# Kernel tuning notes

Measured on AMD Instinct MI355X. Metric: run time of the kernel, lower is better.

Reference implementation:

```python
import jax, jax.numpy as jnp
import numpy as np

D_MODEL = 256
NUM_HEADS = 8
D_HEAD = D_MODEL // NUM_HEADS


def setup_inputs() -> dict:
    key = jax.random.key(0)
    k1, k2, k3, k4, k5, k6 = jax.random.split(key, 6)
    B, L, C, H, W = 2, 2048, D_MODEL, 4, 4
    query = jax.random.normal(k1, (B, L, C, H, W), dtype=jnp.float32)
    key_t = jax.random.normal(k2, (B, L, C, H, W), dtype=jnp.float32)
    value = jax.random.normal(k3, (B, L, C, H, W), dtype=jnp.float32)
    # 1x1 conv weights (out_channels, in_channels), no bias
    s = 1.0 / np.sqrt(C)
    Wq = jax.random.uniform(k4, (C, C), jnp.float32, -s, s)
    Wk = jax.random.uniform(k5, (C, C), jnp.float32, -s, s)
    Wv = jax.random.uniform(k6, (C, C), jnp.float32, -s, s)
    return {"query": query, "key": key_t, "value": value, "Wq": Wq, "Wk": Wk, "Wv": Wv}


def _split_heads(x, B, L, H, W):
    # (B, L, C, H, W) -> (num_heads*B, L, d_head, H, W), head-major like torch permute(2,0,1,3,4,5)
    x = x.reshape(B, L, NUM_HEADS, D_HEAD, H, W)
    x = jnp.transpose(x, (2, 0, 1, 3, 4, 5))  # (nh, B, L, d_head, H, W)
    return x.reshape(NUM_HEADS * B, L, D_HEAD, H, W)


def reference(query, key, value, Wq, Wk, Wv):
    B, L, C, H, W = value.shape
    # 1x1 conv == channel matmul: (B,L,C,H,W) x (O,C) -> (B,L,O,H,W)
    q = jnp.einsum('blchw,oc->blohw', query, Wq)
    k = jnp.einsum('blchw,oc->blohw', key, Wk)
    v = jnp.einsum('blchw,oc->blohw', value, Wv)
    q = _split_heads(q, B, L, H, W)
    k = _split_heads(k, B, L, H, W)
    v = _split_heads(v, B, L, H, W)
    scale = 1.0 / np.sqrt(D_HEAD).astype(np.float32)
    score = jnp.einsum('bidhw,bjdhw->bij', q, k) * scale  # (nh*B, L, L)
    attn = jax.nn.softmax(score, axis=-1)
    context = jnp.einsum('bij,bjdhw->bidhw', attn, v)  # (nh*B, L, d_head, H, W)
    context = context.reshape(NUM_HEADS, B, L, D_HEAD, H, W)
    context = jnp.transpose(context, (1, 2, 0, 3, 4, 5)).reshape(B, L, C, H, W)
    return context, attn
```

## Files before the change

### kernel.cpp

```cpp
#include <hip/hip_runtime.h>


typedef short s16x8 __attribute__((ext_vector_type(8)));
typedef float f32x4 __attribute__((ext_vector_type(4)));

__device__ __forceinline__ unsigned short f2bf(float f) {
  union { float f; unsigned int u; } v; v.f = f;
  return (unsigned short)((v.u + 0x7FFFu + ((v.u >> 16) & 1u)) >> 16);
}
__device__ __forceinline__ float bf2f(unsigned short h) {
  union { unsigned int u; float f; } v; v.u = ((unsigned int)h) << 16;
  return v.f;
}

__device__ __forceinline__ void async_copy16(const unsigned short* g, unsigned short* l) {
  __builtin_amdgcn_global_load_lds((const __attribute__((address_space(1))) void*)g,
                                   (__attribute__((address_space(3))) void*)l, 16, 0, 0);
}


template <int LD>
__device__ __forceinline__ void stage256(const unsigned short* __restrict__ Xg,
                                         unsigned short* __restrict__ lds_base,
                                         int kt) {
  const int tid = threadIdx.x;
  const int wid = tid >> 6, lane = tid & 63;
  const int prow = lane >> 2, pgran = lane & 3;
  const int lgran = pgran ^ ((prow >> 1) & 3);
  const int row0 = wid * 32;
#pragma unroll
  for (int i = 0; i < 2; ++i) {
    const int rb = row0 + i * 16;
    async_copy16(Xg + (size_t)(rb + prow) * LD + kt * 32 + lgran * 8,
                 lds_base + rb * 32);
  }
}

__device__ __forceinline__ void compute256(const unsigned short* __restrict__ As_,
                                           const unsigned short* __restrict__ Bs_,
                                           f32x4 acc[8][4]) {
  const int tid = threadIdx.x, lane = tid & 63, wid = tid >> 6;
  const int wm = wid >> 2, wn = wid & 3;
  const int rl = lane & 15;
  const int xg = (lane >> 4) ^ ((rl >> 1) & 3);
  const unsigned short* Aw = As_ + (size_t)(wm * 128 + rl) * 32 + xg * 8;
  const unsigned short* Bw = Bs_ + (size_t)(wn * 64 + rl) * 32 + xg * 8;
  s16x8 b[4], a[4];
#pragma unroll
  for (int n = 0; n < 4; ++n) b[n] = *(const s16x8*)(Bw + n * 16 * 32);
#pragma unroll
  for (int m = 0; m < 4; ++m) a[m] = *(const s16x8*)(Aw + m * 16 * 32);
  __builtin_amdgcn_s_setprio(1);
#pragma unroll
  for (int m = 0; m < 4; ++m)
#pragma unroll
    for (int n = 0; n < 4; ++n)
      acc[m][n] = __builtin_amdgcn_mfma_f32_16x16x32_bf16(a[m], b[n], acc[m][n], 0, 0, 0);
  __builtin_amdgcn_s_setprio(0);
#pragma unroll
  for (int m = 0; m < 4; ++m) a[m] = *(const s16x8*)(Aw + (64 + m * 16) * 32);
  __builtin_amdgcn_s_setprio(1);
#pragma unroll
  for (int m = 0; m < 4; ++m)
#pragma unroll
    for (int n = 0; n < 4; ++n)
      acc[4 + m][n] = __builtin_amdgcn_mfma_f32_16x16x32_bf16(a[m], b[n], acc[4 + m][n], 0, 0, 0);
  __builtin_amdgcn_s_setprio(0);
}

template <int LD_A, int LD_B, int NT>
__device__ __forceinline__ void gemm256_loop(const unsigned short* __restrict__ Ag,
                                             const unsigned short* __restrict__ Bg,
                                             unsigned short (*As)[8192],
                                             unsigned short (*Bs)[8192],
                                             f32x4 acc[8][4]) {
  stage256<LD_A>(Ag, As[0], 0); stage256<LD_B>(Bg, Bs[0], 0);
  stage256<LD_A>(Ag, As[1], 1); stage256<LD_B>(Bg, Bs[1], 1);
  for (int kt = 0; kt < NT; ++kt) {
    if (kt < NT - 1) asm volatile("s_waitcnt vmcnt(4)" ::: "memory");
    else             asm volatile("s_waitcnt vmcnt(0)" ::: "memory");
    __builtin_amdgcn_s_barrier();
    compute256(As[kt & 1], Bs[kt & 1], acc);
    __builtin_amdgcn_s_barrier();
    if (kt + 2 < NT) {
      stage256<LD_A>(Ag, As[kt & 1], kt + 2);
      stage256<LD_B>(Bg, Bs[kt & 1], kt + 2);
    }
  }
}

#define ACC_INIT8(acc)                        \
  {                                           \
    const f32x4 z_ = {0.f, 0.f, 0.f, 0.f};    \
    _Pragma("unroll")                         \
    for (int m_ = 0; m_ < 8; ++m_)            \
      _Pragma("unroll")                       \
      for (int n_ = 0; n_ < 4; ++n_) acc[m_][n_] = z_; \
  }

__global__ void __launch_bounds__(512, 2)
gemm_proj_qk256_kernel(const unsigned short* __restrict__ Xq,
                       const unsigned short* __restrict__ Xk,
                       const unsigned short* __restrict__ Wbf,
                       unsigned short* __restrict__ q_s,
                       unsigned short* __restrict__ k_s) {
  __shared__ unsigned short As[2][8192], Bs[2][8192];
  f32x4 acc[8][4];
  ACC_INIT8(acc);
  const int z = blockIdx.z;
  const unsigned short* X = z ? Xk : Xq;
  const unsigned short* W = Wbf + z * 65536;
  unsigned short* out = z ? k_s : q_s;
  gemm256_loop<256, 256, 8>(X + (size_t)blockIdx.x * 256 * 256, W, As, Bs, acc);
  const int tid = threadIdx.x, lane = tid & 63, wid = tid >> 6;
  const int wm = wid >> 2, wn = wid & 3;
  const int R0 = blockIdx.x * 256 + wm * 128 + ((lane >> 4) << 2);
  const int C0 = wn * 64 + (lane & 15);
#pragma unroll
  for (int m = 0; m < 8; ++m)
#pragma unroll
    for (int n = 0; n < 4; ++n)
#pragma unroll
      for (int r = 0; r < 4; ++r) {
        int R = R0 + m * 16 + r;
        int o = C0 + n * 16;
        int bl = R >> 4, hw = R & 15;
        int b = bl >> 11, l = bl & 2047;
        int head = o >> 5, d = o & 31;
        out[((size_t)(head * 2 + b) * 2048 + l) * 512 + d * 16 + hw] = f2bf(acc[m][n][r]);
      }
}

__global__ void __launch_bounds__(512, 2)
gemm_proj_vt256_kernel(const unsigned short* __restrict__ W,
                       const unsigned short* __restrict__ X2,
                       unsigned short* __restrict__ vt) {
  __shared__ unsigned short As[2][8192], Bs[2][8192];
  f32x4 acc[8][4];
  ACC_INIT8(acc);
  gemm256_loop<256, 256, 8>(W, X2 + (size_t)blockIdx.x * 256 * 256, As, Bs, acc);
  const int tid = threadIdx.x, lane = tid & 63, wid = tid >> 6;
  const int wm = wid >> 2, wn = wid & 3;
  const int o0 = wm * 128 + ((lane >> 4) << 2);
  const int p0 = blockIdx.x * 256 + wn * 64 + (lane & 15);
#pragma unroll
  for (int m = 0; m < 8; ++m)
#pragma unroll
    for (int n = 0; n < 4; ++n)
#pragma unroll
      for (int r = 0; r < 4; ++r) {
        int o = o0 + m * 16 + r;
        int p = p0 + n * 16;
        int head = o >> 5, d = o & 31;
        int b = p >> 15, hw = (p >> 11) & 15, l = p & 2047;
        vt[((size_t)((head * 2 + b) * 512) + d * 16 + hw) * 2048 + l] = f2bf(acc[m][n][r]);
      }
}

__global__ void __launch_bounds__(512, 2)
gemm_score256_kernel(const unsigned short* __restrict__ q, const unsigned short* __restrict__ k,
                     unsigned short* __restrict__ pbf, float* __restrict__ partial) {
  __shared__ unsigned short As[2][8192], Bs[2][8192];
  f32x4 acc[8][4];
  ACC_INIT8(acc);
  const int bid = blockIdx.x;
  const int w_ = (bid & 7) * 128 + (bid >> 3);
  const int bx = w_ & 7, by = (w_ >> 3) & 7, bh = w_ >> 6;
  const unsigned short* Ag = q + ((size_t)bh * 2048 + bx * 256) * 512;
  const unsigned short* Bg = k + ((size_t)bh * 2048 + by * 256) * 512;
  gemm256_loop<512, 512, 16>(Ag, Bg, As, Bs, acc);
  const int tid = threadIdx.x, lane = tid & 63, wid = tid >> 6;
  const int wm = wid >> 2, wn = wid & 3;
  const float scale = 0.17677669529663687f;
  const int R0 = bx * 256 + wm * 128 + ((lane >> 4) << 2);
  const int C0 = by * 256 + wn * 64 + (lane & 15);
  unsigned short* P = pbf + (size_t)bh * 4194304;
#pragma unroll
  for (int m = 0; m < 8; ++m)
#pragma unroll
    for (int n = 0; n < 4; ++n)
#pragma unroll
      for (int r = 0; r < 4; ++r) {
        float e = __expf(acc[m][n][r] * scale);
        acc[m][n][r] = e;
        P[(size_t)(R0 + m * 16 + r) * 2048 + (C0 + n * 16)] = f2bf(e);
      }
  const int chunk = by * 4 + wn;
#pragma unroll
  for (int m = 0; m < 8; ++m)
#pragma unroll
    for (int r = 0; r < 4; ++r) {
      float s = (acc[m][0][r] + acc[m][1][r]) + (acc[m][2][r] + acc[m][3][r]);
      s += __shfl_xor(s, 1); s += __shfl_xor(s, 2);
      s += __shfl_xor(s, 4); s += __shfl_xor(s, 8);
      if ((lane & 15) == 0)
        partial[((size_t)bh * 2048 + R0 + m * 16 + r) * 32 + chunk] = s;
    }
}

__global__ void __launch_bounds__(512, 2)
gemm_ctx256_kernel(const unsigned short* __restrict__ pbf, const unsigned short* __restrict__ vt,
                   const float* __restrict__ inv_buf, float* __restrict__ outc) {
  __shared__ unsigned short As[2][8192], Bs[2][8192];
  f32x4 acc[8][4];
  ACC_INIT8(acc);
  const int bid = blockIdx.x;
  const int w_ = (bid & 7) * 32 + (bid >> 3);
  const int bx = w_ & 7, by = (w_ >> 3) & 1, bh = w_ >> 4;
  const unsigned short* Ag = pbf + (size_t)bh * 4194304 + (size_t)bx * 256 * 2048;
  const unsigned short* Bg = vt + (size_t)bh * 1048576 + (size_t)by * 256 * 2048;
  gemm256_loop<2048, 2048, 64>(Ag, Bg, As, Bs, acc);
  const int tid = threadIdx.x, lane = tid & 63, wid = tid >> 6;
  const int wm = wid >> 2, wn = wid & 3;
  const int b = bh & 1, head = bh >> 1;
  const int R0 = bx * 256 + wm * 128 + ((lane >> 4) << 2);
  const int C0 = by * 256 + wn * 64 + (lane & 15);
#pragma unroll
  for (int m = 0; m < 8; ++m)
#pragma unroll
    for (int r = 0; r < 4; ++r) {
      const int R = R0 + m * 16 + r;
      const float sc = inv_buf[(size_t)bh * 2048 + R];
#pragma unroll
      for (int n = 0; n < 4; ++n) {
        int dd = C0 + n * 16;
        outc[((size_t)(b * 2048 + R) * 256 + head * 32 + (dd >> 4)) * 16 + (dd & 15)] =
            acc[m][n][r] * sc;
      }
    }
}

__global__ void __launch_bounds__(256) prep_all_kernel(const float* __restrict__ qs,
                                                       const float* __restrict__ ks,
                                                       const float* __restrict__ vs,
                                                       unsigned short* __restrict__ Xq,
                                                       unsigned short* __restrict__ Xk,
                                                       unsigned short* __restrict__ X2) {
  __shared__ float ld[256 * 17];
  const int bl = blockIdx.x;
  const int z = blockIdx.y;
  const int t = threadIdx.x;
  const float* s = (z == 0 ? qs : (z == 1 ? ks : vs)) + (size_t)bl * 4096;
#pragma unroll
  for (int i = 0; i < 4; ++i) {
    int flat = i * 1024 + t * 4;
    float4 v = *(const float4*)(s + flat);
    int c = flat >> 4, hw = flat & 15;
    float* p = &ld[c * 17 + hw];
    p[0] = v.x; p[1] = v.y; p[2] = v.z; p[3] = v.w;
  }
  __syncthreads();
  if (z < 2) {
    unsigned short* d = (z == 0 ? Xq : Xk) + (size_t)bl * 4096;
#pragma unroll
    for (int hw = 0; hw < 16; ++hw)
      d[hw * 256 + t] = f2bf(ld[t * 17 + hw]);
  } else {
    const int b = bl >> 11, l = bl & 2047;
#pragma unroll
    for (int hw = 0; hw < 16; ++hw)
      X2[((size_t)(b * 16 + hw) * 2048 + l) * 256 + t] = f2bf(ld[t * 17 + hw]);
  }
}

__global__ void __launch_bounds__(256) prep_x_kernel(const float* __restrict__ src,
                                                     unsigned short* __restrict__ dst) {
  __shared__ float ld[256 * 17];
  const int bl = blockIdx.x;
  const int t = threadIdx.x;
  const float* s = src + (size_t)bl * 4096;
#pragma unroll
  for (int i = 0; i < 4; ++i) {
    int flat = i * 1024 + t * 4;
    float4 v = *(const float4*)(s + flat);
    int c = flat >> 4, hw = flat & 15;
    float* p = &ld[c * 17 + hw];
    p[0] = v.x; p[1] = v.y; p[2] = v.z; p[3] = v.w;
  }
  __syncthreads();
  unsigned short* d = dst + (size_t)bl * 4096;
#pragma unroll
  for (int hw = 0; hw < 16; ++hw)
    d[hw * 256 + t] = f2bf(ld[t * 17 + hw]);
}

__global__ void __launch_bounds__(256) prep_w_kernel(const float* __restrict__ a,
                                                     const float* __restrict__ b,
                                                     const float* __restrict__ c,
                                                     unsigned short* __restrict__ dst) {
  int i = blockIdx.x * 256 + threadIdx.x;
  const float* s = (i < 65536) ? a : ((i < 131072) ? b : c);
  dst[i] = f2bf(s[i & 65535]);
}

__global__ void __launch_bounds__(256) norm_kernel(const unsigned short* __restrict__ pbf,
                                                   const float* __restrict__ partial,
                                                   float* __restrict__ attn,
                                                   float* __restrict__ inv_buf) {
  __shared__ float sh;
  const int row = blockIdx.x;
  const int t = threadIdx.x;
  if (t < 32) {
    float v = partial[(size_t)row * 32 + t];
    v += __shfl_xor(v, 1); v += __shfl_xor(v, 2);
    v += __shfl_xor(v, 4); v += __shfl_xor(v, 8); v += __shfl_xor(v, 16);
    if (t == 0) sh = v;
  }
  __syncthreads();
  const float inv = 1.0f / sh;
  if (t == 0) inv_buf[row] = inv;
  s16x8 h = *(const s16x8*)(pbf + (size_t)row * 2048 + t * 8);
  float o[8];
#pragma unroll
  for (int i = 0; i < 8; ++i) o[i] = bf2f((unsigned short)h[i]) * inv;
  float* p = attn + (size_t)row * 2048 + t * 8;
  *(float4*)(p)     = *(float4*)&o[0];
  *(float4*)(p + 4) = *(float4*)&o[4];
}

__device__ __forceinline__ void gemm_core_async(const unsigned short* __restrict__ Ag, int ldA,
                                                const unsigned short* __restrict__ Bg, int ldB,
                                                int K, unsigned short* As, unsigned short* Bs,
                                                f32x4 acc[4][4]) {
  const int tid = threadIdx.x;
  const int lane = tid & 63;
  const int w = tid >> 6;
  const int wr = (w >> 1) * 64, wc = (w & 1) * 64;
  const int r = lane >> 2, kk = (lane & 3) * 8;
  for (int k0 = 0; k0 < K; k0 += 32) {
#pragma unroll
    for (int i = 0; i < 2; ++i) {
      const int row0 = w * 32 + i * 16;
      async_copy16(Ag + (size_t)(row0 + r) * ldA + k0 + kk, As + row0 * 32);
      async_copy16(Bg + (size_t)(row0 + r) * ldB + k0 + kk, Bs + row0 * 32);
    }
    __syncthreads();
    s16x8 af[4], bfv[4];
#pragma unroll
    for (int m = 0; m < 4; ++m)
      af[m] = *(const s16x8*)(As + (wr + m * 16 + (lane & 15)) * 32 + (lane >> 4) * 8);
#pragma unroll
    for (int n = 0; n < 4; ++n)
      bfv[n] = *(const s16x8*)(Bs + (wc + n * 16 + (lane & 15)) * 32 + (lane >> 4) * 8);
#pragma unroll
    for (int m = 0; m < 4; ++m)
#pragma unroll
      for (int n = 0; n < 4; ++n)
        acc[m][n] = __builtin_amdgcn_mfma_f32_16x16x32_bf16(af[m], bfv[n], acc[m][n], 0, 0, 0);
    __syncthreads();
  }
}

#define ACC_INIT(acc)                         \
  {                                           \
    const f32x4 z_ = {0.f, 0.f, 0.f, 0.f};    \
    _Pragma("unroll")                         \
    for (int m_ = 0; m_ < 4; ++m_)            \
      _Pragma("unroll")                       \
      for (int n_ = 0; n_ < 4; ++n_) acc[m_][n_] = z_; \
  }

__global__ void __launch_bounds__(256) gemm_proj_kernel(const unsigned short* __restrict__ X,
                                                        const unsigned short* __restrict__ W,
                                                        unsigned short* __restrict__ out) {
  __shared__ unsigned short As[4096], Bs[4096];
  f32x4 acc[4][4];
  ACC_INIT(acc);
  gemm_core_async(X + (size_t)blockIdx.x * 128 * 256, 256,
                  W + (size_t)blockIdx.y * 128 * 256, 256, 256, As, Bs, acc);
  const int tid = threadIdx.x, lane = tid & 63, w = tid >> 6;
  const int wr = (w >> 1) * 64, wc = (w & 1) * 64;
  const int R0 = blockIdx.x * 128 + wr + ((lane >> 4) << 2);
  const int C0 = blockIdx.y * 128 + wc + (lane & 15);
#pragma unroll
  for (int m = 0; m < 4; ++m)
#pragma unroll
    for (int n = 0; n < 4; ++n)
#pragma unroll
      for (int r = 0; r < 4; ++r) {
        int R = R0 + m * 16 + r;
        int o = C0 + n * 16;
        int bl = R >> 4, hw = R & 15;
        int b = bl >> 11, l = bl & 2047;
        int head = o >> 5, d = o & 31;
        out[((size_t)(head * 2 + b) * 2048 + l) * 512 + d * 16 + hw] = f2bf(acc[m][n][r]);
      }
}

__global__ void __launch_bounds__(256) gemm_score_f32_kernel(const unsigned short* __restrict__ q,
                                                             const unsigned short* __restrict__ k,
                                                             float* __restrict__ attn) {
  __shared__ unsigned short As[4096], Bs[4096];
  f32x4 acc[4][4];
  ACC_INIT(acc);
  const int bh = blockIdx.z;
  gemm_core_async(q + ((size_t)bh * 2048 + blockIdx.x * 128) * 512, 512,
                  k + ((size_t)bh * 2048 + blockIdx.y * 128) * 512, 512, 512, As, Bs, acc);
  const int tid = threadIdx.x, lane = tid & 63, w = tid >> 6;
  const int wr = (w >> 1) * 64, wc = (w & 1) * 64;
  float* O = attn + (size_t)bh * 4194304;
  const float scale = 0.17677669529663687f;
  const int R0 = blockIdx.x * 128 + wr + ((lane >> 4) << 2);
  const int C0 = blockIdx.y * 128 + wc + (lane & 15);
#pragma unroll
  for (int m = 0; m < 4; ++m)
#pragma unroll
    for (int n = 0; n < 4; ++n)
#pragma unroll
      for (int r = 0; r < 4; ++r)
        O[(size_t)(R0 + m * 16 + r) * 2048 + (C0 + n * 16)] = acc[m][n][r] * scale;
}

__global__ void __launch_bounds__(256) softmax_kernel(float* __restrict__ attn) {
  __shared__ float red[4];
  float* p = attn + (size_t)blockIdx.x * 2048;
  const int t = threadIdx.x;
  float4 v0 = *(const float4*)(p + t * 8);
  float4 v1 = *(const float4*)(p + t * 8 + 4);
  float mx = fmaxf(fmaxf(fmaxf(v0.x, v0.y), fmaxf(v0.z, v0.w)),
                   fmaxf(fmaxf(v1.x, v1.y), fmaxf(v1.z, v1.w)));
#pragma unroll
  for (int off = 32; off; off >>= 1) mx = fmaxf(mx, __shfl_xor(mx, off));
  if ((t & 63) == 0) red[t >> 6] = mx;
  __syncthreads();
  mx = fmaxf(fmaxf(red[0], red[1]), fmaxf(red[2], red[3]));
  __syncthreads();
  float e[8];
  e[0] = __expf(v0.x - mx); e[1] = __expf(v0.y - mx);
  e[2] = __expf(v0.z - mx); e[3] = __expf(v0.w - mx);
  e[4] = __expf(v1.x - mx); e[5] = __expf(v1.y - mx);
  e[6] = __expf(v1.z - mx); e[7] = __expf(v1.w - mx);
  float s = ((e[0] + e[1]) + (e[2] + e[3])) + ((e[4] + e[5]) + (e[6] + e[7]));
#pragma unroll
  for (int off = 32; off; off >>= 1) s += __shfl_xor(s, off);
  if ((t & 63) == 0) red[t >> 6] = s;
  __syncthreads();
  s = red[0] + red[1] + red[2] + red[3];
  const float inv = 1.0f / s;
  float4 o0 = {e[0] * inv, e[1] * inv, e[2] * inv, e[3] * inv};
  float4 o1 = {e[4] * inv, e[5] * inv, e[6] * inv, e[7] * inv};
  *(float4*)(p + t * 8) = o0;
  *(float4*)(p + t * 8 + 4) = o1;
}

__global__ void __launch_bounds__(256) transpose_v_kernel(const unsigned short* __restrict__ vs,
                                                          unsigned short* __restrict__ vt) {
  __shared__ unsigned short tile[64][65];
  const int bh = blockIdx.z;
  const int j0 = blockIdx.x * 64, d0 = blockIdx.y * 64;
  const unsigned short* src = vs + (size_t)bh * 2048 * 512;
  unsigned short* dst = vt + (size_t)bh * 512 * 2048;
  const int t = threadIdx.x;
#pragma unroll
  for (int i = 0; i < 16; ++i) {
    int e = t * 16 + i;
    int r = e >> 6, c = e & 63;
    tile[r][c] = src[(size_t)(j0 + r) * 512 + d0 + c];
  }
  __syncthreads();
#pragma unroll
  for (int i = 0; i < 16; ++i) {
    int e = t * 16 + i;
    int r = e >> 6, c = e & 63;
    dst[(size_t)(d0 + r) * 2048 + j0 + c] = tile[c][r];
  }
}

__global__ void __launch_bounds__(256) gemm_ctx_f32_kernel(const float* __restrict__ attn,
                                                           const unsigned short* __restrict__ vt,
                                                           float* __restrict__ outc) {
  __shared__ unsigned short As[4096], Bs[4096];
  f32x4 acc[4][4];
  ACC_INIT(acc);
  const int tid = threadIdx.x, lane = tid & 63, w = tid >> 6;
  const int wr = (w >> 1) * 64, wc = (w & 1) * 64;
  const int bh = blockIdx.z;
  const float* Ag = attn + (size_t)bh * 4194304 + (size_t)blockIdx.x * 128 * 2048;
  const unsigned short* Bg = vt + (size_t)bh * 1048576 + (size_t)blockIdx.y * 128 * 2048;
  const int r = lane >> 2, kk = (lane & 3) * 8;
  const int arow = tid >> 1, acol = (tid & 1) * 16;
  for (int k0 = 0; k0 < 2048; k0 += 32) {
#pragma unroll
    for (int i = 0; i < 2; ++i) {
      const int row0 = w * 32 + i * 16;
      async_copy16(Bg + (size_t)(row0 + r) * 2048 + k0 + kk, Bs + row0 * 32);
    }
    {
      const float* sp = Ag + (size_t)arow * 2048 + k0 + acol;
      float4 f0 = *(const float4*)(sp);
      float4 f1 = *(const float4*)(sp + 4);
      float4 f2 = *(const float4*)(sp + 8);
      float4 f3 = *(const float4*)(sp + 12);
      s16x8 h0, h1;
      h0[0] = (short)f2bf(f0.x); h0[1] = (short)f2bf(f0.y);
      h0[2] = (short)f2bf(f0.z); h0[3] = (short)f2bf(f0.w);
      h0[4] = (short)f2bf(f1.x); h0[5] = (short)f2bf(f1.y);
      h0[6] = (short)f2bf(f1.z); h0[7] = (short)f2bf(f1.w);
      h1[0] = (short)f2bf(f2.x); h1[1] = (short)f2bf(f2.y);
      h1[2] = (short)f2bf(f2.z); h1[3] = (short)f2bf(f2.w);
      h1[4] = (short)f2bf(f3.x); h1[5] = (short)f2bf(f3.y);
      h1[6] = (short)f2bf(f3.z); h1[7] = (short)f2bf(f3.w);
      *(s16x8*)(As + arow * 32 + acol) = h0;
      *(s16x8*)(As + arow * 32 + acol + 8) = h1;
    }
    __syncthreads();
    s16x8 af[4], bfv[4];
#pragma unroll
    for (int m = 0; m < 4; ++m)
      af[m] = *(const s16x8*)(As + (wr + m * 16 + (lane & 15)) * 32 + (lane >> 4) * 8);
#pragma unroll
    for (int n = 0; n < 4; ++n)
      bfv[n] = *(const s16x8*)(Bs + (wc + n * 16 + (lane & 15)) * 32 + (lane >> 4) * 8);
#pragma unroll
    for (int m = 0; m < 4; ++m)
#pragma unroll
      for (int n = 0; n < 4; ++n)
        acc[m][n] = __builtin_amdgcn_mfma_f32_16x16x32_bf16(af[m], bfv[n], acc[m][n], 0, 0, 0);
    __syncthreads();
  }
  const int b = bh & 1, head = bh >> 1;
  const int R0 = blockIdx.x * 128 + wr + ((lane >> 4) << 2);
  const int C0 = blockIdx.y * 128 + wc + (lane & 15);
#pragma unroll
  for (int m = 0; m < 4; ++m)
#pragma unroll
    for (int n = 0; n < 4; ++n)
#pragma unroll
      for (int r2 = 0; r2 < 4; ++r2) {
        int R = R0 + m * 16 + r2;
        int dd = C0 + n * 16;
        outc[((size_t)(b * 2048 + R) * 256 + head * 32 + (dd >> 4)) * 16 + (dd & 15)] =
            acc[m][n][r2];
      }
}

extern "C" void kernel_launch(void* const* d_in, const int* in_sizes, int n_in,
                              void* d_out, int out_size, void* d_ws, size_t ws_size,
                              hipStream_t stream) {
  const float* query = (const float*)d_in[0];
  const float* key   = (const float*)d_in[1];
  const float* value = (const float*)d_in[2];
  const float* Wq    = (const float*)d_in[3];
  const float* Wk    = (const float*)d_in[4];
  const float* Wv    = (const float*)d_in[5];

  float* out_ctx  = (float*)d_out;
  float* out_attn = (float*)d_out + 16777216;

  unsigned short* X2   = (unsigned short*)d_ws;
  unsigned short* q_s  = X2 + 16777216;
  unsigned short* k_s  = q_s + 16777216;
  unsigned short* v_t  = k_s + 16777216;
  unsigned short* Wbf  = v_t + 16777216;
  unsigned short* P_bf = Wbf + 196608;
  float* partial = (float*)(P_bf + 67108864);
  float* inv_buf = partial + 1048576;

  unsigned short* Xq = P_bf;
  unsigned short* Xk = P_bf + 16777216;

  const bool fused = ws_size >= (size_t)273154048;

  prep_w_kernel<<<768, 256, 0, stream>>>(Wq, Wk, Wv, Wbf);

  if (fused) {
    prep_all_kernel<<<dim3(4096, 3), 256, 0, stream>>>(query, key, value, Xq, Xk, X2);
    gemm_proj_qk256_kernel<<<dim3(256, 1, 2), 512, 0, stream>>>(Xq, Xk, Wbf, q_s, k_s);
    gemm_proj_vt256_kernel<<<dim3(256, 1, 1), 512, 0, stream>>>(Wbf + 131072, X2, v_t);
    gemm_score256_kernel<<<1024, 512, 0, stream>>>(q_s, k_s, P_bf, partial);
    norm_kernel<<<32768, 256, 0, stream>>>(P_bf, partial, out_attn, inv_buf);
    gemm_ctx256_kernel<<<256, 512, 0, stream>>>(P_bf, v_t, inv_buf, out_ctx);
  } else {
    prep_x_kernel<<<4096, 256, 0, stream>>>(query, X2);
    gemm_proj_kernel<<<dim3(512, 2), 256, 0, stream>>>(X2, Wbf, q_s);
    prep_x_kernel<<<4096, 256, 0, stream>>>(key, X2);
    gemm_proj_kernel<<<dim3(512, 2), 256, 0, stream>>>(X2, Wbf + 65536, k_s);
    prep_x_kernel<<<4096, 256, 0, stream>>>(value, X2);
    gemm_proj_kernel<<<dim3(512, 2), 256, 0, stream>>>(X2, Wbf + 131072, v_t);
    gemm_score_f32_kernel<<<dim3(16, 16, 16), 256, 0, stream>>>(q_s, k_s, out_attn);
    softmax_kernel<<<32768, 256, 0, stream>>>(out_attn);
    transpose_v_kernel<<<dim3(32, 8, 16), 256, 0, stream>>>(v_t, X2);
    gemm_ctx_f32_kernel<<<dim3(16, 4, 16), 256, 0, stream>>>(out_attn, X2, out_ctx);
  }
}
```

Baseline: 422.6 us.

## Merge projection GEMMs and overlap attn normalization with context GEMM

Combines the Q/K and V projection GEMMs into one 768-block launch, so the V blocks fill the GPU alongside the Q/K ones. Splits the row-sum reduction into a small inv_kernel, then runs the attn normalization write (reading the bf16 P and writing fp32 attn) as extra blocks in the same grid as the context GEMM. The aim is to overlap the bandwidth-bound attn write with the compute-bound context GEMM and to cut launch gaps. Risks: the GEMM blocks sit at the start of the grid and may be scheduled unevenly, and launch_bounds of 4 blocks per CU could pressure registers in the GEMM path.

```diff
diff --git a/kernel.cpp b/kernel.cpp
--- a/kernel.cpp
+++ b/kernel.cpp
@@ -99,62 +99,58 @@
   }
 
 __global__ void __launch_bounds__(512, 2)
-gemm_proj_qk256_kernel(const unsigned short* __restrict__ Xq,
+gemm_proj_fused_kernel(const unsigned short* __restrict__ Xq,
                        const unsigned short* __restrict__ Xk,
                        const unsigned short* __restrict__ Wbf,
+                       const unsigned short* __restrict__ X2,
                        unsigned short* __restrict__ q_s,
-                       unsigned short* __restrict__ k_s) {
-  __shared__ unsigned short As[2][8192], Bs[2][8192];
-  f32x4 acc[8][4];
-  ACC_INIT8(acc);
-  const int z = blockIdx.z;
-  const unsigned short* X = z ? Xk : Xq;
-  const unsigned short* W = Wbf + z * 65536;
-  unsigned short* out = z ? k_s : q_s;
-  gemm256_loop<256, 256, 8>(X + (size_t)blockIdx.x * 256 * 256, W, As, Bs, acc);
-  const int tid = threadIdx.x, lane = tid & 63, wid = tid >> 6;
-  const int wm = wid >> 2, wn = wid & 3;
-  const int R0 = blockIdx.x * 256 + wm * 128 + ((lane >> 4) << 2);
-  const int C0 = wn * 64 + (lane & 15);
-#pragma unroll
-  for (int m = 0; m < 8; ++m)
-#pragma unroll
-    for (int n = 0; n < 4; ++n)
-#pragma unroll
-      for (int r = 0; r < 4; ++r) {
-        int R = R0 + m * 16 + r;
-        int o = C0 + n * 16;
-        int bl = R >> 4, hw = R & 15;
-        int b = bl >> 11, l = bl & 2047;
-        int head = o >> 5, d = o & 31;
-        out[((size_t)(head * 2 + b) * 2048 + l) * 512 + d * 16 + hw] = f2bf(acc[m][n][r]);
-      }
-}
-
-__global__ void __launch_bounds__(512, 2)
-gemm_proj_vt256_kernel(const unsigned short* __restrict__ W,
-                       const unsigned short* __restrict__ X2,
+                       unsigned short* __restrict__ k_s,
                        unsigned short* __restrict__ vt) {
   __shared__ unsigned short As[2][8192], Bs[2][8192];
   f32x4 acc[8][4];
   ACC_INIT8(acc);
-  gemm256_loop<256, 256, 8>(W, X2 + (size_t)blockIdx.x * 256 * 256, As, Bs, acc);
+  const int bid = blockIdx.x;
   const int tid = threadIdx.x, lane = tid & 63, wid = tid >> 6;
   const int wm = wid >> 2, wn = wid & 3;
-  const int o0 = wm * 128 + ((lane >> 4) << 2);
-  const int p0 = blockIdx.x * 256 + wn * 64 + (lane & 15);
-#pragma unroll
-  for (int m = 0; m < 8; ++m)
-#pragma unroll
-    for (int n = 0; n < 4; ++n)
-#pragma unroll
-      for (int r = 0; r < 4; ++r) {
-        int o = o0 + m * 16 + r;
-        int p = p0 + n * 16;
-        int head = o >> 5, d = o & 31;
-        int b = p >> 15, hw = (p >> 11) & 15, l = p & 2047;
-        vt[((size_t)((head * 2 + b) * 512) + d * 16 + hw) * 2048 + l] = f2bf(acc[m][n][r]);
-      }
+  if (bid < 512) {
+    const int z = bid >> 8, bx = bid & 255;
+    const unsigned short* X = z ? Xk : Xq;
+    const unsigned short* W = Wbf + z * 65536;
+    unsigned short* out = z ? k_s : q_s;
+    gemm256_loop<256, 256, 8>(X + (size_t)bx * 65536, W, As, Bs, acc);
+    const int R0 = bx * 256 + wm * 128 + ((lane >> 4) << 2);
+    const int C0 = wn * 64 + (lane & 15);
+#pragma unroll
+    for (int m = 0; m < 8; ++m)
+#pragma unroll
+      for (int n = 0; n < 4; ++n)
+#pragma unroll
+        for (int r = 0; r < 4; ++r) {
+          int R = R0 + m * 16 + r;
+          int o = C0 + n * 16;
+          int bl = R >> 4, hw = R & 15;
+          int b = bl >> 11, l = bl & 2047;
+          int head = o >> 5, d = o & 31;
+          out[((size_t)(head * 2 + b) * 2048 + l) * 512 + d * 16 + hw] = f2bf(acc[m][n][r]);
+        }
+  } else {
+    const int bx = bid - 512;
+    gemm256_loop<256, 256, 8>(Wbf + 131072, X2 + (size_t)bx * 65536, As, Bs, acc);
+    const int o0 = wm * 128 + ((lane >> 4) << 2);
+    const int p0 = bx * 256 + wn * 64 + (lane & 15);
+#pragma unroll
+    for (int m = 0; m < 8; ++m)
+#pragma unroll
+      for (int n = 0; n < 4; ++n)
+#pragma unroll
+        for (int r = 0; r < 4; ++r) {
+          int o = o0 + m * 16 + r;
+          int p = p0 + n * 16;
+          int head = o >> 5, d = o & 31;
+          int b = p >> 15, hw = (p >> 11) & 15, l = p & 2047;
+          vt[((size_t)((head * 2 + b) * 512) + d * 16 + hw) * 2048 + l] = f2bf(acc[m][n][r]);
+        }
+  }
 }
 
 __global__ void __launch_bounds__(512, 2)
@@ -198,19 +194,47 @@
     }
 }
 
-__global__ void __launch_bounds__(512, 2)
-gemm_ctx256_kernel(const unsigned short* __restrict__ pbf, const unsigned short* __restrict__ vt,
-                   const float* __restrict__ inv_buf, float* __restrict__ outc) {
+__global__ void __launch_bounds__(256) inv_kernel(const float* __restrict__ partial,
+                                                  float* __restrict__ inv_buf) {
+  const int t = threadIdx.x;
+  const int row = blockIdx.x * 64 + (t >> 2);
+  const int q4 = t & 3;
+  const float4* p = (const float4*)(partial + (size_t)row * 32 + q4 * 8);
+  float4 a = p[0], b = p[1];
+  float s = ((a.x + a.y) + (a.z + a.w)) + ((b.x + b.y) + (b.z + b.w));
+  s += __shfl_xor(s, 1); s += __shfl_xor(s, 2);
+  if (q4 == 0) inv_buf[row] = 1.0f / s;
+}
+
+__global__ void __launch_bounds__(512, 4)
+gemm_ctx_norm_kernel(const unsigned short* __restrict__ pbf, const unsigned short* __restrict__ vt,
+                     const float* __restrict__ inv_buf, float* __restrict__ attn,
+                     float* __restrict__ outc) {
   __shared__ unsigned short As[2][8192], Bs[2][8192];
+  const int bid = blockIdx.x;
+  const int tid = threadIdx.x;
+  if (bid >= 256) {
+    const int nb = bid - 256;
+    const int row = nb * 2 + (tid >> 8);
+    const int t = tid & 255;
+    const float inv = inv_buf[row];
+    s16x8 h = *(const s16x8*)(pbf + (size_t)row * 2048 + t * 8);
+    float o[8];
+#pragma unroll
+    for (int i = 0; i < 8; ++i) o[i] = bf2f((unsigned short)h[i]) * inv;
+    float* p = attn + (size_t)row * 2048 + t * 8;
+    *(float4*)(p)     = *(float4*)&o[0];
+    *(float4*)(p + 4) = *(float4*)&o[4];
+    return;
+  }
   f32x4 acc[8][4];
   ACC_INIT8(acc);
-  const int bid = blockIdx.x;
   const int w_ = (bid & 7) * 32 + (bid >> 3);
   const int bx = w_ & 7, by = (w_ >> 3) & 1, bh = w_ >> 4;
   const unsigned short* Ag = pbf + (size_t)bh * 4194304 + (size_t)bx * 256 * 2048;
   const unsigned short* Bg = vt + (size_t)bh * 1048576 + (size_t)by * 256 * 2048;
   gemm256_loop<2048, 2048, 64>(Ag, Bg, As, Bs, acc);
-  const int tid = threadIdx.x, lane = tid & 63, wid = tid >> 6;
+  const int lane = tid & 63, wid = tid >> 6;
   const int wm = wid >> 2, wn = wid & 3;
   const int b = bh & 1, head = bh >> 1;
   const int R0 = bx * 256 + wm * 128 + ((lane >> 4) << 2);
@@ -291,31 +315,6 @@
   int i = blockIdx.x * 256 + threadIdx.x;
   const float* s = (i < 65536) ? a : ((i < 131072) ? b : c);
   dst[i] = f2bf(s[i & 65535]);
-}
-
-__global__ void __launch_bounds__(256) norm_kernel(const unsigned short* __restrict__ pbf,
-                                                   const float* __restrict__ partial,
-                                                   float* __restrict__ attn,
-                                                   float* __restrict__ inv_buf) {
-  __shared__ float sh;
-  const int row = blockIdx.x;
-  const int t = threadIdx.x;
-  if (t < 32) {
-    float v = partial[(size_t)row * 32 + t];
-    v += __shfl_xor(v, 1); v += __shfl_xor(v, 2);
-    v += __shfl_xor(v, 4); v += __shfl_xor(v, 8); v += __shfl_xor(v, 16);
-    if (t == 0) sh = v;
-  }
-  __syncthreads();
-  const float inv = 1.0f / sh;
-  if (t == 0) inv_buf[row] = inv;
-  s16x8 h = *(const s16x8*)(pbf + (size_t)row * 2048 + t * 8);
-  float o[8];
-#pragma unroll
-  for (int i = 0; i < 8; ++i) o[i] = bf2f((unsigned short)h[i]) * inv;
-  float* p = attn + (size_t)row * 2048 + t * 8;
-  *(float4*)(p)     = *(float4*)&o[0];
-  *(float4*)(p + 4) = *(float4*)&o[4];
 }
 
 __device__ __forceinline__ void gemm_core_async(const unsigned short* __restrict__ Ag, int ldA,
@@ -565,11 +564,10 @@
 
   if (fused) {
     prep_all_kernel<<<dim3(4096, 3), 256, 0, stream>>>(query, key, value, Xq, Xk, X2);
-    gemm_proj_qk256_kernel<<<dim3(256, 1, 2), 512, 0, stream>>>(Xq, Xk, Wbf, q_s, k_s);
-    gemm_proj_vt256_kernel<<<dim3(256, 1, 1), 512, 0, stream>>>(Wbf + 131072, X2, v_t);
+    gemm_proj_fused_kernel<<<768, 512, 0, stream>>>(Xq, Xk, Wbf, X2, q_s, k_s, v_t);
     gemm_score256_kernel<<<1024, 512, 0, stream>>>(q_s, k_s, P_bf, partial);
-    norm_kernel<<<32768, 256, 0, stream>>>(P_bf, partial, out_attn, inv_buf);
-    gemm_ctx256_kernel<<<256, 512, 0, stream>>>(P_bf, v_t, inv_buf, out_ctx);
+    inv_kernel<<<512, 256, 0, stream>>>(partial, inv_buf);
+    gemm_ctx_norm_kernel<<<16640, 512, 0, stream>>>(P_bf, v_t, inv_buf, out_attn, out_ctx);
   } else {
     prep_x_kernel<<<4096, 256, 0, stream>>>(query, X2);
     gemm_proj_kernel<<<dim3(512, 2), 256, 0, stream>>>(X2, Wbf, q_s);
```

Result: slower. 934.7 us (+121.2%).
